# Performance work log

Measured on AMD Instinct MI355X. Metric: run time of the kernel, lower is better.

## Reference

```python
import jax, jax.numpy as jnp
import numpy as np

HIDDEN = 2560
N_HEADS = 32
HEAD_DIM = HIDDEN // N_HEADS  # 80
ROPE_PCT = 0.25
ROT = int(HEAD_DIM * ROPE_PCT)  # 20
THETA = 10000.0


def setup_inputs() -> dict:
    key = jax.random.key(0)
    ks = jax.random.split(key, 6)
    B, S = 2, 2048
    hidden_states = jax.random.normal(ks[0], (B, S, HIDDEN), dtype=jnp.float32)
    attention_mask = jnp.ones((B, S), dtype=jnp.float32)  # unused in no-cache path
    position_ids = jnp.tile(jnp.arange(S, dtype=jnp.int32)[None, :], (B, 1))
    scale = 1.0 / np.sqrt(HIDDEN)
    Wq = jax.random.normal(ks[1], (HIDDEN, HIDDEN), dtype=jnp.float32) * scale
    Wk = jax.random.normal(ks[2], (HIDDEN, HIDDEN), dtype=jnp.float32) * scale
    Wv = jax.random.normal(ks[3], (HIDDEN, HIDDEN), dtype=jnp.float32) * scale
    Wo = jax.random.normal(ks[4], (HIDDEN, HIDDEN), dtype=jnp.float32) * scale
    return {"hidden_states": hidden_states, "attention_mask": attention_mask,
            "position_ids": position_ids, "Wq": Wq, "Wk": Wk, "Wv": Wv, "Wo": Wo}


def _rotate_half(x):
    x1, x2 = jnp.split(x, 2, axis=-1)
    return jnp.concatenate([-x2, x1], axis=-1)


def _rope_cos_sin(position_ids, dtype):
    # inv_freq over rotary dims
    inv_freq = 1.0 / (THETA ** (jnp.arange(0, ROT, 2, dtype=jnp.float32) / ROT))
    pos = position_ids.astype(jnp.float32)  # [B,S]
    freqs = pos[..., None] * inv_freq[None, None, :]  # [B,S,ROT/2]
    emb = jnp.concatenate([freqs, freqs], axis=-1)    # [B,S,ROT]
    cos = jnp.cos(emb)[:, None, :, :].astype(dtype)   # [B,1,S,ROT]
    sin = jnp.sin(emb)[:, None, :, :].astype(dtype)
    return cos, sin


def reference(hidden_states, attention_mask, position_ids, Wq, Wk, Wv, Wo):
    B, S, H = hidden_states.shape
    dtype = hidden_states.dtype
    # projections: [B,S,H] -> [B,nh,S,hd]
    def split_heads(x):
        return x.reshape(B, S, N_HEADS, HEAD_DIM).transpose(0, 2, 1, 3)
    q = split_heads(hidden_states @ Wq)
    k = split_heads(hidden_states @ Wk)
    v = split_heads(hidden_states @ Wv)

    # partial RoPE on first ROT dims
    cos, sin = _rope_cos_sin(position_ids, dtype)
    q_rot, q_pass = q[..., :ROT], q[..., ROT:]
    k_rot, k_pass = k[..., :ROT], k[..., ROT:]
    q_rot = q_rot * cos + _rotate_half(q_rot) * sin
    k_rot = k_rot * cos + _rotate_half(k_rot) * sin
    q = jnp.concatenate([q_rot, q_pass], axis=-1)
    k = jnp.concatenate([k_rot, k_pass], axis=-1)

    # causal attention (no KV cache -> is_causal=True SDPA path)
    scale = 1.0 / np.sqrt(HEAD_DIM)
    scores = jnp.einsum("bhqd,bhkd->bhqk", q, k) * scale
    causal = jnp.tril(jnp.ones((S, S), dtype=bool))
    scores = jnp.where(causal[None, None, :, :], scores, jnp.finfo(jnp.float32).min)
    probs = jax.nn.softmax(scores.astype(jnp.float32), axis=-1).astype(dtype)
    attn = jnp.einsum("bhqk,bhkd->bhqd", probs, v)
    attn = attn.transpose(0, 2, 1, 3).reshape(B, S, H)
    return attn @ Wo
```

## Files before the change

### kernel.cpp

```cpp
#include <hip/hip_runtime.h>
#include <stdint.h>

typedef unsigned short u16;
typedef __bf16 bf16x8 __attribute__((ext_vector_type(8)));
typedef float floatx4 __attribute__((ext_vector_type(4)));

#define HIDDEN 2560
#define NHEADS 32
#define HD 80
#define SEQ 2048
#define BATCH 2
#define MROWS (BATCH*SEQ)
#define QB 64

__device__ __forceinline__ float bf2f(uint32_t bits) {
    return __uint_as_float(bits << 16);
}
__device__ __forceinline__ u16 f2bf_bits(float f) {
    uint32_t x = __float_as_uint(f);
    uint32_t r = (x + 0x7fffu + ((x >> 16) & 1u)) >> 16;
    return (u16)r;
}
__device__ __forceinline__ floatx4 mk4(float x) {
    return (floatx4){x, x, x, x};
}
__device__ __forceinline__ floatx4 exp4(floatx4 a) {
    floatx4 r;
#pragma unroll
    for (int i = 0; i < 4; i++) r[i] = __expf(a[i]);
    return r;
}
__device__ __forceinline__ void gload16(const u16* g, u16* l) {
    __builtin_amdgcn_global_load_lds(
        (const __attribute__((address_space(1))) uint32_t*)g,
        (__attribute__((address_space(3))) uint32_t*)l, 16, 0, 0);
}

__global__ __launch_bounds__(256) void split_x(const float* __restrict__ in,
                                               u16* __restrict__ hi,
                                               u16* __restrict__ lo,
                                               float scale) {
    size_t i4 = (size_t)blockIdx.x * 256 + threadIdx.x;
    float4 v = ((const float4*)in)[i4];
    float f[4] = {v.x * scale, v.y * scale, v.z * scale, v.w * scale};
    u16 h[4], l[4];
#pragma unroll
    for (int j = 0; j < 4; j++) {
        h[j] = f2bf_bits(f[j]);
        l[j] = f2bf_bits(f[j] - bf2f(h[j]));
    }
    ((uint2*)hi)[i4] = *(uint2*)h;
    ((uint2*)lo)[i4] = *(uint2*)l;
}

__global__ __launch_bounds__(256) void split_wt(const float* __restrict__ in,
                                                u16* __restrict__ outh,
                                                u16* __restrict__ outl) {
    __shared__ float t[64][65];
    int k0 = blockIdx.x * 64;
    int n0 = blockIdx.y * 64;
    int tid = threadIdx.x;
    int rr = tid >> 4;
    int c4 = (tid & 15) * 4;
#pragma unroll
    for (int it = 0; it < 4; it++) {
        int row = it * 16 + rr;
        float4 v = *(const float4*)&in[(size_t)(k0 + row) * HIDDEN + n0 + c4];
        t[row][c4 + 0] = v.x; t[row][c4 + 1] = v.y;
        t[row][c4 + 2] = v.z; t[row][c4 + 3] = v.w;
    }
    __syncthreads();
#pragma unroll
    for (int it = 0; it < 4; it++) {
        int row = it * 16 + rr;
        float f[4] = { t[c4 + 0][row], t[c4 + 1][row], t[c4 + 2][row], t[c4 + 3][row] };
        u16 h[4], l[4];
#pragma unroll
        for (int j = 0; j < 4; j++) {
            h[j] = f2bf_bits(f[j]);
            l[j] = f2bf_bits(f[j] - bf2f(h[j]));
        }
        size_t o = (size_t)(n0 + row) * HIDDEN + k0 + c4;
        *(uint2*)&outh[o] = *(uint2*)h;
        *(uint2*)&outl[o] = *(uint2*)l;
    }
}

__global__ __launch_bounds__(256) void gemm_bt2(const u16* __restrict__ Ah,
                                                const u16* __restrict__ Al,
                                                const u16* __restrict__ Bh,
                                                const u16* __restrict__ Bl,
                                                float* __restrict__ C) {
    __shared__ u16 lds[2 * 16384];
    const int K = HIDDEN;
    int tid  = threadIdx.x;
    int lane = tid & 63;
    int wave = tid >> 6;
    int wr = wave >> 1, wc = wave & 1;
    int lr = lane & 15, lq = lane >> 4;

    int nwgx = gridDim.x;
    int orig = blockIdx.y * nwgx + blockIdx.x;
    int cpx  = (nwgx * gridDim.y) >> 3;
    int wg   = (orig & 7) * cpx + (orig >> 3);
    int n0 = (wg % nwgx) * 128, m0 = (wg / nwgx) * 128;

    int srow = wave * 32 + (lane >> 2);
    int scol = ((lane & 3) ^ ((lane >> 3) & 3)) * 8;
    const u16* gAh = Ah + (size_t)(m0 + srow) * K + scol;
    const u16* gAl = Al + (size_t)(m0 + srow) * K + scol;
    const u16* gBh = Bh + (size_t)(n0 + srow) * K + scol;
    const u16* gBl = Bl + (size_t)(n0 + srow) * K + scol;
    const size_t q1 = (size_t)16 * K;
    int dso = wave * 1024;

    floatx4 acc[4][4];
#pragma unroll
    for (int i = 0; i < 4; i++)
#pragma unroll
        for (int j = 0; j < 4; j++)
            acc[i][j] = mk4(0.f);

    int swz = (lr >> 1) & 3;
    int rsl = (lq ^ swz) * 8;

    auto stage = [&](int k0, int bsel) {
        u16* Bf = lds + bsel * 16384 + dso;
        gload16(gAh + k0, Bf);          gload16(gAh + q1 + k0, Bf + 512);
        gload16(gAl + k0, Bf + 4096);   gload16(gAl + q1 + k0, Bf + 4608);
        gload16(gBh + k0, Bf + 8192);   gload16(gBh + q1 + k0, Bf + 8704);
        gload16(gBl + k0, Bf + 12288);  gload16(gBl + q1 + k0, Bf + 12800);
    };

    const int NT = K / 32;
    stage(0, 0);
    for (int t = 0; t < NT; t++) {
        __syncthreads();
        if (t + 1 < NT) stage((t + 1) * 32, (t + 1) & 1);
        u16* Bc = lds + (t & 1) * 16384;
        bf16x8 ah[4], al[4], bh[4], bl[4];
#pragma unroll
        for (int i = 0; i < 4; i++) {
            int ra = (wr * 64 + i * 16 + lr) * 32 + rsl;
            int rb = (wc * 64 + i * 16 + lr) * 32 + rsl;
            ah[i] = *(const bf16x8*)&Bc[ra];
            al[i] = *(const bf16x8*)&Bc[4096 + ra];
            bh[i] = *(const bf16x8*)&Bc[8192 + rb];
            bl[i] = *(const bf16x8*)&Bc[12288 + rb];
        }
#pragma unroll
        for (int i = 0; i < 4; i++)
#pragma unroll
            for (int j = 0; j < 4; j++) {
                acc[i][j] = __builtin_amdgcn_mfma_f32_16x16x32_bf16(ah[i], bh[j], acc[i][j], 0, 0, 0);
                acc[i][j] = __builtin_amdgcn_mfma_f32_16x16x32_bf16(ah[i], bl[j], acc[i][j], 0, 0, 0);
                acc[i][j] = __builtin_amdgcn_mfma_f32_16x16x32_bf16(al[i], bh[j], acc[i][j], 0, 0, 0);
            }
    }
#pragma unroll
    for (int i = 0; i < 4; i++) {
        int rowb = m0 + wr * 64 + i * 16 + lq * 4;
#pragma unroll
        for (int j = 0; j < 4; j++) {
            int col = n0 + wc * 64 + j * 16 + lr;
#pragma unroll
            for (int r = 0; r < 4; r++)
                C[(size_t)(rowb + r) * HIDDEN + col] = acc[i][j][r];
        }
    }
}

__global__ __launch_bounds__(256) void rope_k(float* __restrict__ Qb, float* __restrict__ Kb,
                                              const int* __restrict__ pos_ids) {
    int idx = blockIdx.x * 256 + threadIdx.x;
    int row = idx >> 5;
    int h   = idx & 31;
    float pos = (float)pos_ids[row];
    size_t base = (size_t)row * HIDDEN + h * HD;
    float* q = Qb + base;
    float* k = Kb + base;
#pragma unroll
    for (int i = 0; i < 10; i++) {
        float freq = pos * exp2f(-1.3287712379549449f * (float)i);
        float sn, cs;
        sincosf(freq, &sn, &cs);
        float q1 = q[i], q2 = q[i + 10];
        q[i]      = q1 * cs - q2 * sn;
        q[i + 10] = q2 * cs + q1 * sn;
        float k1 = k[i], k2 = k[i + 10];
        k[i]      = k1 * cs - k2 * sn;
        k[i + 10] = k2 * cs + k1 * sn;
    }
}

__global__ __launch_bounds__(256) void vtrans(const float* __restrict__ Vb,
                                              u16* __restrict__ Vth,
                                              u16* __restrict__ Vtl) {
    __shared__ float t[64][81];
    int bh = blockIdx.x; int b = bh >> 5, h = bh & 31;
    int s0 = blockIdx.y * 64;
    int tid = threadIdx.x;
    for (int idx = tid; idx < 64 * 20; idx += 256) {
        int s = idx / 20, c = idx % 20;
        float4 v = *(const float4*)&Vb[(size_t)(b * SEQ + s0 + s) * HIDDEN + h * HD + c * 4];
        t[s][c * 4 + 0] = v.x; t[s][c * 4 + 1] = v.y;
        t[s][c * 4 + 2] = v.z; t[s][c * 4 + 3] = v.w;
    }
    __syncthreads();
    for (int idx = tid; idx < 80 * 16; idx += 256) {
        int d = idx >> 4, ch = idx & 15;
        int t2 = ch >> 3, e = ch & 7, a = e >> 1, h2 = e & 1;
        int srck = t2 * 32 + 16 * h2 + 4 * a;
        int dstc = t2 * 32 + 8 * a + 4 * h2;
        u16 hh[4], ll[4];
#pragma unroll
        for (int j = 0; j < 4; j++) {
            float f = t[srck + j][d];
            hh[j] = f2bf_bits(f);
            ll[j] = f2bf_bits(f - bf2f(hh[j]));
        }
        size_t o = ((size_t)bh * HD + d) * SEQ + s0 + dstc;
        *(uint2*)&Vth[o] = *(uint2*)hh;
        *(uint2*)&Vtl[o] = *(uint2*)ll;
    }
}

__global__ __launch_bounds__(256, 4) void attn_mfma(const u16* __restrict__ Qh_,
                                                 const u16* __restrict__ Ql_,
                                                 const u16* __restrict__ Kh_,
                                                 const u16* __restrict__ Kl_,
                                                 const u16* __restrict__ Vth_,
                                                 const u16* __restrict__ Vtl_,
                                                 u16* __restrict__ Oh_,
                                                 u16* __restrict__ Ol_) {
    __shared__ u16 lds[20480];

    int tid = threadIdx.x;
    int lane = tid & 63, w = tid >> 6;
    int lr = lane & 15, lq = lane >> 4;
    int bh = blockIdx.x; int b = bh >> 5, h = bh & 31;
    int qblk = (gridDim.y - 1) - blockIdx.y;
    int q0 = qblk * QB;
    size_t rowbase = (size_t)b * SEQ;
    size_t hoff = (size_t)h * HD;

    bf16x8 qh[2], ql[2], qta;
    for (int idx = tid; idx < 1280; idx += 256) {
        int buf = idx >= 640; int e = idx - buf * 640;
        int r = e / 10, c = e % 10;
        const u16* src = (buf ? Ql_ : Qh_) +
            (rowbase + q0 + r) * HIDDEN + hoff + c * 8;
        *(int4*)&lds[buf * 6656 + r * 104 + c * 8] = *(const int4*)src;
    }
    __syncthreads();
    {
        int tba = (lq >> 1) ? 6656 : 0;
        int tcol = 64 + (lq & 1) * 8;
        int lrow = w * 16 + lr;
#pragma unroll
        for (int c = 0; c < 2; c++) {
            qh[c] = *(const bf16x8*)&lds[lrow * 104 + c * 32 + lq * 8];
            ql[c] = *(const bf16x8*)&lds[6656 + lrow * 104 + c * 32 + lq * 8];
        }
        qta = *(const bf16x8*)&lds[tba + lrow * 104 + tcol];
    }
    __syncthreads();

    floatx4 acc[5];
    float mrow = -3.0e38f, lsum = 0.f;
#pragma unroll
    for (int nt = 0; nt < 5; nt++) acc[nt] = mk4(0.f);

    int ntiles = 2 * qblk + 2;
    int qw0 = q0 + w * 16;

    int k0RowOff = (lane >> 3) * HIDDEN + (((lane & 7) ^ (lane >> 3)) * 8);
    int k1RowOff = (lane >> 1) * HIDDEN + 64 + (lane & 1) * 8;
    int vRowOff  = (lane >> 2) * SEQ + ((((lane & 3) ^ ((lane >> 3) & 3))) * 8);
    const u16* kSrc = (w & 1 ? Kl_ : Kh_) + rowbase * HIDDEN + hoff;
    const u16* vSrc = (w == 3 ? Vtl_ : Vth_) + (size_t)bh * HD * SEQ;

    auto stage = [&](int t, int bsel) {
        int k0 = t * 32;
        u16* B = lds + bsel * 10240;
        if (w < 2) {
            const u16* kb = kSrc + (size_t)k0 * HIDDEN;
            u16* d0 = B + w * 2048;
#pragma unroll
            for (int j = 0; j < 4; j++)
                gload16(kb + (size_t)j * 8 * HIDDEN + k0RowOff, d0 + j * 512);
            gload16(kb + k1RowOff, B + 4096 + w * 512);
        } else {
            const u16* vb = vSrc + k0;
            u16* d0 = B + 5120 + (w == 3 ? 2560 : 0);
#pragma unroll
            for (int j = 0; j < 5; j++)
                gload16(vb + (size_t)j * 16 * SEQ + vRowOff, d0 + j * 512);
        }
    };

    int ks0 = ((lq) ^ (lr & 7)) * 8;
    int ks1 = ((4 + lq) ^ (lr & 7)) * 8;
    int k1off  = (lq >> 1) * 512 + (lq & 1) * 8;
    int k1offb = ((lq >> 1) ^ 1) * 512 + (lq & 1) * 8;
    int vsl = (lq ^ ((lr >> 1) & 3)) * 8;

    stage(0, 0);

    for (int t = 0; t < ntiles; t++) {
        int k0 = t * 32;
        __syncthreads();
        if (t + 1 < ntiles) stage(t + 1, (t + 1) & 1);
        u16* B = lds + (t & 1) * 10240;
        if (k0 <= qw0 + 15) {
            u16* bK0h = B;
            u16* bK0l = B + 2048;
            u16* bK1  = B + 4096;
            u16* bVh  = B + 5120;
            u16* bVl  = B + 7680;
            __builtin_amdgcn_s_setprio(1);
            floatx4 s[2];
#pragma unroll
            for (int st = 0; st < 2; st++) {
                int krow = st * 16 + lr;
                bf16x8 kh0 = *(const bf16x8*)&bK0h[krow * 64 + ks0];
                bf16x8 kh1 = *(const bf16x8*)&bK0h[krow * 64 + ks1];
                bf16x8 kl0 = *(const bf16x8*)&bK0l[krow * 64 + ks0];
                bf16x8 kl1 = *(const bf16x8*)&bK0l[krow * 64 + ks1];
                bf16x8 k1f  = *(const bf16x8*)&bK1[krow * 16 + k1off];
                bf16x8 k1fb = *(const bf16x8*)&bK1[krow * 16 + k1offb];
                floatx4 sv = mk4(0.f);
                sv = __builtin_amdgcn_mfma_f32_16x16x32_bf16(kh0, qh[0], sv, 0, 0, 0);
                sv = __builtin_amdgcn_mfma_f32_16x16x32_bf16(kl0, qh[0], sv, 0, 0, 0);
                sv = __builtin_amdgcn_mfma_f32_16x16x32_bf16(kh0, ql[0], sv, 0, 0, 0);
                sv = __builtin_amdgcn_mfma_f32_16x16x32_bf16(kh1, qh[1], sv, 0, 0, 0);
                sv = __builtin_amdgcn_mfma_f32_16x16x32_bf16(kl1, qh[1], sv, 0, 0, 0);
                sv = __builtin_amdgcn_mfma_f32_16x16x32_bf16(kh1, ql[1], sv, 0, 0, 0);
                sv = __builtin_amdgcn_mfma_f32_16x16x32_bf16(k1f,  qta, sv, 0, 0, 0);
                sv = __builtin_amdgcn_mfma_f32_16x16x32_bf16(k1fb, qta, sv, 0, 0, 0);
                s[st] = sv;
            }
            if (k0 + 31 > qw0) {
                int qmy = qw0 + lr - k0 - lq * 4;
#pragma unroll
                for (int r = 0; r < 4; r++) {
                    s[0][r] = (r <= qmy)      ? s[0][r] : -3.0e38f;
                    s[1][r] = (16 + r <= qmy) ? s[1][r] : -3.0e38f;
                }
            }
            float rm = fmaxf(fmaxf(fmaxf(s[0][0], s[0][1]), fmaxf(s[0][2], s[0][3])),
                             fmaxf(fmaxf(s[1][0], s[1][1]), fmaxf(s[1][2], s[1][3])));
            rm = fmaxf(rm, __shfl_xor(rm, 16));
            rm = fmaxf(rm, __shfl_xor(rm, 32));
            int need = rm > mrow + 8.f;
            if (__any(need)) {
                float mnew = fmaxf(mrow, rm);
                float alpha = __expf(mrow - mnew);
                mrow = mnew;
                lsum *= alpha;
                float at[4];
#pragma unroll
                for (int r = 0; r < 4; r++) at[r] = __shfl(alpha, lq * 4 + r);
#pragma unroll
                for (int nt = 0; nt < 5; nt++)
#pragma unroll
                    for (int r = 0; r < 4; r++) acc[nt][r] *= at[r];
            }
            floatx4 p0 = exp4(s[0] - mk4(mrow));
            floatx4 p1 = exp4(s[1] - mk4(mrow));
            floatx4 ps = p0 + p1;
            float rs = ps[0] + ps[1] + ps[2] + ps[3];
            rs += __shfl_xor(rs, 16);
            rs += __shfl_xor(rs, 32);
            lsum += rs;
            bf16x8 pa;
            pa[0] = (__bf16)p0[0]; pa[1] = (__bf16)p0[1];
            pa[2] = (__bf16)p0[2]; pa[3] = (__bf16)p0[3];
            pa[4] = (__bf16)p1[0]; pa[5] = (__bf16)p1[1];
            pa[6] = (__bf16)p1[2]; pa[7] = (__bf16)p1[3];
#pragma unroll
            for (int nt = 0; nt < 5; nt++) {
                bf16x8 vh = *(const bf16x8*)&bVh[(nt * 16 + lr) * 32 + vsl];
                bf16x8 vl = *(const bf16x8*)&bVl[(nt * 16 + lr) * 32 + vsl];
                acc[nt] = __builtin_amdgcn_mfma_f32_16x16x32_bf16(pa, vh, acc[nt], 0, 0, 0);
                acc[nt] = __builtin_amdgcn_mfma_f32_16x16x32_bf16(pa, vl, acc[nt], 0, 0, 0);
            }
            __builtin_amdgcn_s_setprio(0);
        }
    }
    {
        float il = 1.f / lsum;
        float inv[4];
#pragma unroll
        for (int r = 0; r < 4; r++) inv[r] = __shfl(il, lq * 4 + r);
#pragma unroll
        for (int nt = 0; nt < 5; nt++) {
#pragma unroll
            for (int r = 0; r < 4; r++) {
                float o = acc[nt][r] * inv[r];
                u16 hh = f2bf_bits(o);
                u16 ll = f2bf_bits(o - bf2f(hh));
                size_t row = rowbase + qw0 + lq * 4 + r;
                Oh_[row * HIDDEN + hoff + nt * 16 + lr] = hh;
                Ol_[row * HIDDEN + hoff + nt * 16 + lr] = ll;
            }
        }
    }
}

extern "C" void kernel_launch(void* const* d_in, const int* in_sizes, int n_in,
                              void* d_out, int out_size, void* d_ws, size_t ws_size,
                              hipStream_t stream) {
    const float* hidden = (const float*)d_in[0];
    const int* pos    = (const int*)d_in[2];
    const float* Wq   = (const float*)d_in[3];
    const float* Wk   = (const float*)d_in[4];
    const float* Wv   = (const float*)d_in[5];
    const float* Wo   = (const float*)d_in[6];

    const size_t NQ = (size_t)MROWS * HIDDEN;
    float* ws = (float*)d_ws;
    float* Qb = ws;
    float* Kb = ws + NQ;
    float* Vb = ws + 2 * NQ;
    u16* Ah  = (u16*)(ws + 3 * NQ);
    u16* Al  = Ah + NQ;
    u16* WTh = Al + NQ;
    u16* WTl = WTh + (size_t)HIDDEN * HIDDEN;
    u16* Vth = Ah;
    u16* Vtl = Al;
    u16* Qh  = (u16*)Vb;
    u16* Ql  = Qh + NQ;
    u16* Kh  = (u16*)Qb;
    u16* Kl  = Kh + NQ;
    u16* Oh  = (u16*)Kb;
    u16* Ol  = Oh + NQ;

    const float SC = 0.11180339887498949f;

    dim3 blk(256);
    dim3 wgrid(HIDDEN / 64, HIDDEN / 64);
    dim3 ggrid(HIDDEN / 128, MROWS / 128);

    split_x<<<dim3(NQ / 1024), blk, 0, stream>>>(hidden, Ah, Al, 1.f);
    split_wt<<<wgrid, blk, 0, stream>>>(Wq, WTh, WTl);
    gemm_bt2<<<ggrid, blk, 0, stream>>>(Ah, Al, WTh, WTl, Qb);
    split_wt<<<wgrid, blk, 0, stream>>>(Wk, WTh, WTl);
    gemm_bt2<<<ggrid, blk, 0, stream>>>(Ah, Al, WTh, WTl, Kb);
    split_wt<<<wgrid, blk, 0, stream>>>(Wv, WTh, WTl);
    gemm_bt2<<<ggrid, blk, 0, stream>>>(Ah, Al, WTh, WTl, Vb);
    rope_k<<<dim3(MROWS * NHEADS / 256), blk, 0, stream>>>(Qb, Kb, pos);
    vtrans<<<dim3(BATCH * NHEADS, SEQ / 64), blk, 0, stream>>>(Vb, Vth, Vtl);
    split_x<<<dim3(NQ / 1024), blk, 0, stream>>>(Qb, Qh, Ql, SC);
    split_x<<<dim3(NQ / 1024), blk, 0, stream>>>(Kb, Kh, Kl, 1.f);
    attn_mfma<<<dim3(BATCH * NHEADS, SEQ / QB), blk, 0, stream>>>(Qh, Ql, Kh, Kl,
                                                                  Vth, Vtl, Oh, Ol);
    split_wt<<<wgrid, blk, 0, stream>>>(Wo, WTh, WTl);
    gemm_bt2<<<ggrid, blk, 0, stream>>>(Oh, Ol, WTh, WTl, (float*)d_out);
}
```

Baseline: 1.177 ms.

## Fuse V transpose/split into GEMM epilogue and RoPE with bf16 split

The V projection GEMM now writes the transposed, hi/lo bf16-split V layout straight from its epilogue, which removes the fp32 V buffer round trip and the separate vtrans kernel. RoPE is fused with the hi/lo split and the scaling, so Q and K are each read once and written as bf16 pairs. Workspace aliasing is rearranged so the buffers do not collide. The GEMM epilogue stores become scattered 8-byte writes, and rope_split keeps 80 floats per thread in registers, which may reduce occupancy.

```diff
diff --git a/kernel.cpp b/kernel.cpp
--- a/kernel.cpp
+++ b/kernel.cpp
@@ -170,58 +170,141 @@
     }
 }
 
-__global__ __launch_bounds__(256) void rope_k(float* __restrict__ Qb, float* __restrict__ Kb,
-                                              const int* __restrict__ pos_ids) {
+__global__ __launch_bounds__(256) void gemm_bt2v(const u16* __restrict__ Ah,
+                                                 const u16* __restrict__ Al,
+                                                 const u16* __restrict__ Bh,
+                                                 const u16* __restrict__ Bl,
+                                                 u16* __restrict__ Vth,
+                                                 u16* __restrict__ Vtl) {
+    __shared__ u16 lds[2 * 16384];
+    const int K = HIDDEN;
+    int tid  = threadIdx.x;
+    int lane = tid & 63;
+    int wave = tid >> 6;
+    int wr = wave >> 1, wc = wave & 1;
+    int lr = lane & 15, lq = lane >> 4;
+
+    int nwgx = gridDim.x;
+    int orig = blockIdx.y * nwgx + blockIdx.x;
+    int cpx  = (nwgx * gridDim.y) >> 3;
+    int wg   = (orig & 7) * cpx + (orig >> 3);
+    int n0 = (wg % nwgx) * 128, m0 = (wg / nwgx) * 128;
+
+    int srow = wave * 32 + (lane >> 2);
+    int scol = ((lane & 3) ^ ((lane >> 3) & 3)) * 8;
+    const u16* gAh = Ah + (size_t)(m0 + srow) * K + scol;
+    const u16* gAl = Al + (size_t)(m0 + srow) * K + scol;
+    const u16* gBh = Bh + (size_t)(n0 + srow) * K + scol;
+    const u16* gBl = Bl + (size_t)(n0 + srow) * K + scol;
+    const size_t q1 = (size_t)16 * K;
+    int dso = wave * 1024;
+
+    floatx4 acc[4][4];
+#pragma unroll
+    for (int i = 0; i < 4; i++)
+#pragma unroll
+        for (int j = 0; j < 4; j++)
+            acc[i][j] = mk4(0.f);
+
+    int swz = (lr >> 1) & 3;
+    int rsl = (lq ^ swz) * 8;
+
+    auto stage = [&](int k0, int bsel) {
+        u16* Bf = lds + bsel * 16384 + dso;
+        gload16(gAh + k0, Bf);          gload16(gAh + q1 + k0, Bf + 512);
+        gload16(gAl + k0, Bf + 4096);   gload16(gAl + q1 + k0, Bf + 4608);
+        gload16(gBh + k0, Bf + 8192);   gload16(gBh + q1 + k0, Bf + 8704);
+        gload16(gBl + k0, Bf + 12288);  gload16(gBl + q1 + k0, Bf + 12800);
+    };
+
+    const int NT = K / 32;
+    stage(0, 0);
+    for (int t = 0; t < NT; t++) {
+        __syncthreads();
+        if (t + 1 < NT) stage((t + 1) * 32, (t + 1) & 1);
+        u16* Bc = lds + (t & 1) * 16384;
+        bf16x8 ah[4], al[4], bh[4], bl[4];
+#pragma unroll
+        for (int i = 0; i < 4; i++) {
+            int ra = (wr * 64 + i * 16 + lr) * 32 + rsl;
+            int rb = (wc * 64 + i * 16 + lr) * 32 + rsl;
+            ah[i] = *(const bf16x8*)&Bc[ra];
+            al[i] = *(const bf16x8*)&Bc[4096 + ra];
+            bh[i] = *(const bf16x8*)&Bc[8192 + rb];
+            bl[i] = *(const bf16x8*)&Bc[12288 + rb];
+        }
+#pragma unroll
+        for (int i = 0; i < 4; i++)
+#pragma unroll
+            for (int j = 0; j < 4; j++) {
+                acc[i][j] = __builtin_amdgcn_mfma_f32_16x16x32_bf16(ah[i], bh[j], acc[i][j], 0, 0, 0);
+                acc[i][j] = __builtin_amdgcn_mfma_f32_16x16x32_bf16(ah[i], bl[j], acc[i][j], 0, 0, 0);
+                acc[i][j] = __builtin_amdgcn_mfma_f32_16x16x32_bf16(al[i], bh[j], acc[i][j], 0, 0, 0);
+            }
+    }
+#pragma unroll
+    for (int i = 0; i < 4; i++) {
+        int rowb = m0 + wr * 64 + i * 16 + lq * 4;
+        int b    = rowb >> 11;
+        int srw  = rowb & (SEQ - 1);
+        int kbase = (srw & ~31) + 8 * ((srw >> 2) & 3) + 4 * ((srw >> 4) & 1);
+#pragma unroll
+        for (int j = 0; j < 4; j++) {
+            int col = n0 + wc * 64 + j * 16 + lr;
+            int h = col / HD;
+            int d = col - h * HD;
+            size_t o = ((size_t)(b * NHEADS + h) * HD + d) * SEQ + kbase;
+            u16 hh[4], ll[4];
+#pragma unroll
+            for (int r = 0; r < 4; r++) {
+                float f = acc[i][j][r];
+                hh[r] = f2bf_bits(f);
+                ll[r] = f2bf_bits(f - bf2f(hh[r]));
+            }
+            *(uint2*)&Vth[o] = *(uint2*)hh;
+            *(uint2*)&Vtl[o] = *(uint2*)ll;
+        }
+    }
+}
+
+__global__ __launch_bounds__(256) void rope_split(const float* __restrict__ src,
+                                                  const int* __restrict__ pos_ids,
+                                                  u16* __restrict__ oh,
+                                                  u16* __restrict__ ol,
+                                                  float scale) {
     int idx = blockIdx.x * 256 + threadIdx.x;
     int row = idx >> 5;
     int h   = idx & 31;
     float pos = (float)pos_ids[row];
     size_t base = (size_t)row * HIDDEN + h * HD;
-    float* q = Qb + base;
-    float* k = Kb + base;
+    const float* p = src + base;
+    float v[80];
+#pragma unroll
+    for (int c = 0; c < 20; c++) {
+        float4 q = *(const float4*)&p[c * 4];
+        v[c * 4 + 0] = q.x; v[c * 4 + 1] = q.y;
+        v[c * 4 + 2] = q.z; v[c * 4 + 3] = q.w;
+    }
 #pragma unroll
     for (int i = 0; i < 10; i++) {
         float freq = pos * exp2f(-1.3287712379549449f * (float)i);
         float sn, cs;
         sincosf(freq, &sn, &cs);
-        float q1 = q[i], q2 = q[i + 10];
-        q[i]      = q1 * cs - q2 * sn;
-        q[i + 10] = q2 * cs + q1 * sn;
-        float k1 = k[i], k2 = k[i + 10];
-        k[i]      = k1 * cs - k2 * sn;
-        k[i + 10] = k2 * cs + k1 * sn;
-    }
-}
-
-__global__ __launch_bounds__(256) void vtrans(const float* __restrict__ Vb,
-                                              u16* __restrict__ Vth,
-                                              u16* __restrict__ Vtl) {
-    __shared__ float t[64][81];
-    int bh = blockIdx.x; int b = bh >> 5, h = bh & 31;
-    int s0 = blockIdx.y * 64;
-    int tid = threadIdx.x;
-    for (int idx = tid; idx < 64 * 20; idx += 256) {
-        int s = idx / 20, c = idx % 20;
-        float4 v = *(const float4*)&Vb[(size_t)(b * SEQ + s0 + s) * HIDDEN + h * HD + c * 4];
-        t[s][c * 4 + 0] = v.x; t[s][c * 4 + 1] = v.y;
-        t[s][c * 4 + 2] = v.z; t[s][c * 4 + 3] = v.w;
-    }
-    __syncthreads();
-    for (int idx = tid; idx < 80 * 16; idx += 256) {
-        int d = idx >> 4, ch = idx & 15;
-        int t2 = ch >> 3, e = ch & 7, a = e >> 1, h2 = e & 1;
-        int srck = t2 * 32 + 16 * h2 + 4 * a;
-        int dstc = t2 * 32 + 8 * a + 4 * h2;
+        float q1 = v[i], q2 = v[i + 10];
+        v[i]      = q1 * cs - q2 * sn;
+        v[i + 10] = q2 * cs + q1 * sn;
+    }
+#pragma unroll
+    for (int c = 0; c < 20; c++) {
         u16 hh[4], ll[4];
 #pragma unroll
-        for (int j = 0; j < 4; j++) {
-            float f = t[srck + j][d];
-            hh[j] = f2bf_bits(f);
-            ll[j] = f2bf_bits(f - bf2f(hh[j]));
-        }
-        size_t o = ((size_t)bh * HD + d) * SEQ + s0 + dstc;
-        *(uint2*)&Vth[o] = *(uint2*)hh;
-        *(uint2*)&Vtl[o] = *(uint2*)ll;
+        for (int r = 0; r < 4; r++) {
+            float f = v[c * 4 + r] * scale;
+            hh[r] = f2bf_bits(f);
+            ll[r] = f2bf_bits(f - bf2f(hh[r]));
+        }
+        *(uint2*)&oh[base + c * 4] = *(uint2*)hh;
+        *(uint2*)&ol[base + c * 4] = *(uint2*)ll;
     }
 }
 
@@ -427,10 +510,10 @@
     u16* Al  = Ah + NQ;
     u16* WTh = Al + NQ;
     u16* WTl = WTh + (size_t)HIDDEN * HIDDEN;
-    u16* Vth = Ah;
-    u16* Vtl = Al;
-    u16* Qh  = (u16*)Vb;
-    u16* Ql  = Qh + NQ;
+    u16* Vth = (u16*)Vb;
+    u16* Vtl = Vth + NQ;
+    u16* Qh  = Ah;
+    u16* Ql  = Al;
     u16* Kh  = (u16*)Qb;
     u16* Kl  = Kh + NQ;
     u16* Oh  = (u16*)Kb;
@@ -448,11 +531,9 @@
     split_wt<<<wgrid, blk, 0, stream>>>(Wk, WTh, WTl);
     gemm_bt2<<<ggrid, blk, 0, stream>>>(Ah, Al, WTh, WTl, Kb);
     split_wt<<<wgrid, blk, 0, stream>>>(Wv, WTh, WTl);
-    gemm_bt2<<<ggrid, blk, 0, stream>>>(Ah, Al, WTh, WTl, Vb);
-    rope_k<<<dim3(MROWS * NHEADS / 256), blk, 0, stream>>>(Qb, Kb, pos);
-    vtrans<<<dim3(BATCH * NHEADS, SEQ / 64), blk, 0, stream>>>(Vb, Vth, Vtl);
-    split_x<<<dim3(NQ / 1024), blk, 0, stream>>>(Qb, Qh, Ql, SC);
-    split_x<<<dim3(NQ / 1024), blk, 0, stream>>>(Kb, Kh, Kl, 1.f);
+    gemm_bt2v<<<ggrid, blk, 0, stream>>>(Ah, Al, WTh, WTl, Vth, Vtl);
+    rope_split<<<dim3(MROWS * NHEADS / 256), blk, 0, stream>>>(Qb, pos, Qh, Ql, SC);
+    rope_split<<<dim3(MROWS * NHEADS / 256), blk, 0, stream>>>(Kb, pos, Kh, Kl, 1.f);
     attn_mfma<<<dim3(BATCH * NHEADS, SEQ / QB), blk, 0, stream>>>(Qh, Ql, Kh, Kl,
                                                                   Vth, Vtl, Oh, Ol);
     split_wt<<<wgrid, blk, 0, stream>>>(Wo, WTh, WTl);
```

Result: faster. 1.138 ms (-3.3%).
